# Kernel tuning notes

Measured on AMD Instinct MI355X. Metric: run time of the kernel, lower is better.

## Reference

```python
import jax, jax.numpy as jnp
import numpy as np

V, E, L, H = 128, 512, 8, 8
B, T = 4, 1024
EPS = 0.1  # label smoothing


def _ln(x, s, b):
    mu = x.mean(-1, keepdims=True)
    var = ((x - mu) ** 2).mean(-1, keepdims=True)
    return (x - mu) * jax.lax.rsqrt(var + 1e-5) * s + b


def _forward(inputs, targets, emb, qkv_w, qkv_b, aff1_w, aff1_b, aff2_w, aff2_b,
             ffn1_w, ffn1_b, ffn2_w, ffn2_b, ln1_s, ln1_b, ln2_s, ln2_b, head_w, head_b):
    Bx, Tx = inputs.shape
    x = emb[inputs]                                  # [B,T,E]
    dh = E // H
    mask = jnp.tril(jnp.ones((Tx, Tx), dtype=x.dtype))
    scale = np.float32(1.0 / np.sqrt(dh))
    for l in range(L):
        qkv = x @ qkv_w[l].T + qkv_b[l]              # [B,T,3E]
        qkv = qkv.reshape(Bx, Tx, H, 3 * dh).transpose(0, 2, 1, 3)  # [B,H,T,3dh]
        q, k, v = jnp.split(qkv, 3, axis=-1)
        # NOTE: original multiplies scores by boolean tril mask (zeros, not -inf)
        scores = jnp.einsum('bhqd,bhkd->bhqk', q, k) * mask * scale
        att = jax.nn.softmax(scores, axis=-1) @ v    # [B,H,T,dh]
        att = att.transpose(0, 2, 1, 3).reshape(Bx, Tx, E)
        att = jax.nn.relu(att @ aff1_w[l].T + aff1_b[l]) @ aff2_w[l].T + aff2_b[l]
        out1 = _ln(att + x, ln1_s[l], ln1_b[l])
        out2 = jax.nn.relu(out1 @ ffn1_w[l].T + ffn1_b[l]) @ ffn2_w[l].T + ffn2_b[l]
        x = _ln(out1 + out2, ln2_s[l], ln2_b[l])
    logits = x @ head_w.T + head_b                   # [B,T,V]
    logp = jax.nn.log_softmax(logits, axis=-1)
    nll = -jnp.take_along_axis(logp, targets[..., None], axis=-1)[..., 0]
    smooth = -logp.mean(-1)
    loss = jnp.mean((1.0 - EPS) * nll + EPS * smooth)
    return logits, loss


def setup_inputs() -> dict:
    key = jax.random.key(0)
    ks = jax.random.split(key, 16)
    s = lambda k, shape, fan: (jax.random.normal(k, shape, jnp.float32) / np.sqrt(fan)).astype(jnp.float32)
    return {
        'inputs': jax.random.randint(ks[0], (B, T), 0, V, dtype=jnp.int32).astype(jnp.int64),
        'targets': jax.random.randint(ks[1], (B, T), 0, V, dtype=jnp.int32).astype(jnp.int64),
        'emb': s(ks[2], (V, E), 1.0),
        'qkv_w': s(ks[3], (L, 3 * E, E), E),
        'qkv_b': jnp.zeros((L, 3 * E), jnp.float32),
        'aff1_w': s(ks[4], (L, E, E), E),
        'aff1_b': jnp.zeros((L, E), jnp.float32),
        'aff2_w': s(ks[5], (L, E, E), E),
        'aff2_b': jnp.zeros((L, E), jnp.float32),
        'ffn1_w': s(ks[6], (L, E, E), E),
        'ffn1_b': jnp.zeros((L, E), jnp.float32),
        'ffn2_w': s(ks[7], (L, E, E), E),
        'ffn2_b': jnp.zeros((L, E), jnp.float32),
        'ln1_s': jnp.ones((L, E), jnp.float32),
        'ln1_b': jnp.zeros((L, E), jnp.float32),
        'ln2_s': jnp.ones((L, E), jnp.float32),
        'ln2_b': jnp.zeros((L, E), jnp.float32),
        'head_w': s(ks[8], (V, E), E),
        'head_b': jnp.zeros((V,), jnp.float32),
    }


def reference(inputs, targets, emb, qkv_w, qkv_b, aff1_w, aff1_b, aff2_w, aff2_b,
              ffn1_w, ffn1_b, ffn2_w, ffn2_b, ln1_s, ln1_b, ln2_s, ln2_b, head_w, head_b):
    return _forward(inputs, targets, emb, qkv_w, qkv_b, aff1_w, aff1_b, aff2_w, aff2_b,
                    ffn1_w, ffn1_b, ffn2_w, ffn2_b, ln1_s, ln1_b, ln2_s, ln2_b, head_w, head_b)
```

## Files before the change

### kernel.cpp

```cpp
#include <hip/hip_runtime.h>


#define V_  128
#define E_  512
#define L_  8
#define H_  8
#define B_  4
#define T_  1024
#define N_  (B_*T_)
#define DH_ 64
#define E3_ 1536

typedef __attribute__((ext_vector_type(8))) short   bf16x8;
typedef __attribute__((ext_vector_type(4))) float   floatx4;

#define SW(row,k8) (((row) << 6) + ((((k8) ^ ((row) & 7))) << 3))

__device__ __forceinline__ unsigned short f2bf(float f) {
    union { float f; unsigned int i; } v; v.f = f;
    unsigned int x = v.i;
    return (unsigned short)((x + 0x7fffu + ((x >> 16) & 1u)) >> 16);
}
__device__ __forceinline__ float bf2f(unsigned short u) {
    union { unsigned int i; float f; } v; v.i = ((unsigned int)u) << 16; return v.f;
}
__device__ __forceinline__ void gload_lds16(const void* g, void* l) {
    __builtin_amdgcn_global_load_lds(
        (const __attribute__((address_space(1))) unsigned int*)g,
        (__attribute__((address_space(3))) unsigned int*)l, 16, 0, 0);
}

__device__ __forceinline__ void xcd_remap(int& mstrip, int& nblk) {
    int nx = gridDim.x;
    int flat = blockIdx.y * nx + blockIdx.x;
    int xcd = flat & 7;
    int j = flat >> 3;
    int per_xcd = gridDim.y >> 3;
    mstrip = xcd * per_xcd + j / nx;
    nblk = j % nx;
}

#define CVT_N0 6291456
#define CVT_N1 2097152
#define CVT_TOT (CVT_N0 + 4*CVT_N1 + V_*E_)
__global__ void cvt_all_kernel(const float* __restrict__ s0, const float* __restrict__ s1,
                               const float* __restrict__ s2, const float* __restrict__ s3,
                               const float* __restrict__ s4, const float* __restrict__ s5,
                               unsigned short* __restrict__ dst) {
    long i = (long)(blockIdx.x * blockDim.x + threadIdx.x) * 4;
    if (i >= CVT_TOT) return;
    const float* src; long off;
    if      (i < CVT_N0)               { src = s0; off = i; }
    else if (i < CVT_N0 + CVT_N1)      { src = s1; off = i - CVT_N0; }
    else if (i < CVT_N0 + 2*CVT_N1)    { src = s2; off = i - CVT_N0 - CVT_N1; }
    else if (i < CVT_N0 + 3*CVT_N1)    { src = s3; off = i - CVT_N0 - 2L*CVT_N1; }
    else if (i < CVT_N0 + 4*CVT_N1)    { src = s4; off = i - CVT_N0 - 3L*CVT_N1; }
    else                               { src = s5; off = i - CVT_N0 - 4L*CVT_N1; }
    float4 v = *(const float4*)(src + off);
    ushort4 o; o.x = f2bf(v.x); o.y = f2bf(v.y); o.z = f2bf(v.z); o.w = f2bf(v.w);
    *(ushort4*)(dst + i) = o;
}

__global__ void embed_kernel(const int* __restrict__ tok, const float* __restrict__ emb,
                             float* __restrict__ xf, unsigned short* __restrict__ xb) {
    int idx = blockIdx.x * blockDim.x + threadIdx.x;
    if (idx >= N_ * E_) return;
    int n = idx >> 9;
    int e = idx & (E_ - 1);
    float v = emb[tok[n] * E_ + e];
    xf[idx] = v; xb[idx] = f2bf(v);
}

template<int RELU, int WF, int WB, int ADDRES>
__global__ __launch_bounds__(256) void gemm64(
    const unsigned short* __restrict__ A, const unsigned short* __restrict__ W,
    const float* __restrict__ bias, const float* __restrict__ resF,
    float* __restrict__ Cf, unsigned short* __restrict__ Cb,
    int M, int Nout, int K)
{
    __shared__ unsigned short Asm[4][64 * 64];
    __shared__ unsigned short Bsm[4][64 * 64];
    int tid = threadIdx.x;
    int wv = tid >> 6, ln = tid & 63;
    int lquad = ln >> 4, lmod = ln & 15;
    int mh = wv & 1, kh = wv >> 1;
    int mstrip, nblk;
    xcd_remap(mstrip, nblk);
    int m0 = mstrip * 64, n0 = nblk * 64;

    floatx4 acc[2][4] = {};

    auto stage = [&](int k0, int s) {
        #pragma unroll
        for (int c = 0; c < 2; ++c) {
            int cc = tid + 256 * c;
            int r = cc >> 3, k8s = (cc & 7) ^ (r & 7);
            gload_lds16(A + (size_t)(m0 + r) * K + k0 + 8 * k8s,
                        &Asm[s][2048 * c + 512 * wv]);
        }
        #pragma unroll
        for (int c = 0; c < 2; ++c) {
            int cc = tid + 256 * c;
            int r = cc >> 3, k8s = (cc & 7) ^ (r & 7);
            gload_lds16(W + (size_t)(n0 + r) * K + k0 + 8 * k8s,
                        &Bsm[s][2048 * c + 512 * wv]);
        }
    };

    int np = K >> 7;
    stage(0, 0);
    stage(64, 1);
    __syncthreads();

    for (int t = 0; t < np; ++t) {
        if (t + 1 < np) {
            stage((2 * t + 2) << 6, (2 * t + 2) & 3);
            stage((2 * t + 3) << 6, (2 * t + 3) & 3);
        }
        #pragma unroll
        for (int half = 0; half < 2; ++half) {
            int s = (2 * t + half) & 3;
            bf16x8 af[2], bfr[4];
            #pragma unroll
            for (int i = 0; i < 2; ++i)
                af[i] = *(const bf16x8*)&Asm[s][SW(32 * mh + 16 * i + lmod, 4 * kh + lquad)];
            #pragma unroll
            for (int j = 0; j < 4; ++j)
                bfr[j] = *(const bf16x8*)&Bsm[s][SW(16 * j + lmod, 4 * kh + lquad)];
            #pragma unroll
            for (int i = 0; i < 2; ++i)
                #pragma unroll
                for (int j = 0; j < 4; ++j)
                    acc[i][j] = __builtin_amdgcn_mfma_f32_16x16x32_bf16(af[i], bfr[j], acc[i][j], 0, 0, 0);
        }
        if (t + 1 < np) __syncthreads();
    }

    float* redF = (float*)&Asm[0][0];
    if (kh == 1) {
        #pragma unroll
        for (int i = 0; i < 2; ++i)
            #pragma unroll
            for (int j = 0; j < 4; ++j) {
                int bidx = i * 4 + j;
                *(floatx4*)&redF[mh * 2048 + ln * 32 + (((bidx ^ (ln & 7))) << 2)] = acc[i][j];
            }
    }
    __syncthreads();
    if (kh == 0) {
        #pragma unroll
        for (int i = 0; i < 2; ++i)
            #pragma unroll
            for (int j = 0; j < 4; ++j) {
                int bidx = i * 4 + j;
                floatx4 part = *(const floatx4*)&redF[mh * 2048 + ln * 32 + (((bidx ^ (ln & 7))) << 2)];
                int n = n0 + 16 * j + lmod;
                float bj = bias[n];
                #pragma unroll
                for (int v = 0; v < 4; ++v) {
                    int m = m0 + 32 * mh + 16 * i + 4 * lquad + v;
                    float val = acc[i][j][v] + part[v] + bj;
                    if (ADDRES) val += resF[(size_t)m * Nout + n];
                    if (RELU) val = fmaxf(val, 0.f);
                    if (WF) Cf[(size_t)m * Nout + n] = val;
                    if (WB) Cb[(size_t)m * Nout + n] = f2bf(val);
                }
            }
    }
}

__global__ __launch_bounds__(256) void gemm_qkv(
    const unsigned short* __restrict__ A, const unsigned short* __restrict__ W,
    const float* __restrict__ bias, unsigned short* __restrict__ Cb,
    unsigned short* __restrict__ vt_g, float* __restrict__ vtile, int K)
{
    __shared__ unsigned short Asm[2][128 * 64];
    __shared__ unsigned short Bsm[2][64 * 64];
    __shared__ float vred[4][64];
    int tid = threadIdx.x;
    int wv = tid >> 6, ln = tid & 63;
    int lquad = ln >> 4, lmod = ln & 15;
    int mstrip, nblk;
    xcd_remap(mstrip, nblk);
    int m0 = mstrip * 128, n0 = nblk * 64;

    floatx4 acc[2][4] = {};

    auto stage = [&](int k0, int pb) {
        #pragma unroll
        for (int c = 0; c < 4; ++c) {
            int cc = tid + 256 * c;
            int r = cc >> 3, k8s = (cc & 7) ^ (r & 7);
            gload_lds16(A + (size_t)(m0 + r) * K + k0 + 8 * k8s,
                        &Asm[pb][2048 * c + 512 * wv]);
        }
        #pragma unroll
        for (int c = 0; c < 2; ++c) {
            int cc = tid + 256 * c;
            int r = cc >> 3, k8s = (cc & 7) ^ (r & 7);
            gload_lds16(W + (size_t)(n0 + r) * K + k0 + 8 * k8s,
                        &Bsm[pb][2048 * c + 512 * wv]);
        }
    };

    int nt = K >> 6;
    stage(0, 0);
    __syncthreads();
    for (int t = 0; t < nt; ++t) {
        int pb = t & 1;
        if (t + 1 < nt) stage((t + 1) << 6, pb ^ 1);
        #pragma unroll
        for (int ks = 0; ks < 2; ++ks) {
            bf16x8 af[2], bfr[4];
            #pragma unroll
            for (int i = 0; i < 2; ++i)
                af[i] = *(const bf16x8*)&Asm[pb][SW(32 * wv + 16 * i + lmod, ks * 4 + lquad)];
            #pragma unroll
            for (int j = 0; j < 4; ++j)
                bfr[j] = *(const bf16x8*)&Bsm[pb][SW(16 * j + lmod, ks * 4 + lquad)];
            #pragma unroll
            for (int i = 0; i < 2; ++i)
                #pragma unroll
                for (int j = 0; j < 4; ++j)
                    acc[i][j] = __builtin_amdgcn_mfma_f32_16x16x32_bf16(af[i], bfr[j], acc[i][j], 0, 0, 0);
        }
        if (t + 1 < nt) __syncthreads();
    }

    if ((n0 % 192) != 128) {
        #pragma unroll
        for (int i = 0; i < 2; ++i)
            #pragma unroll
            for (int j = 0; j < 4; ++j) {
                int n = n0 + 16 * j + lmod;
                float bj = bias[n];
                #pragma unroll
                for (int v = 0; v < 4; ++v) {
                    int m = m0 + 32 * wv + 16 * i + 4 * lquad + v;
                    Cb[(size_t)m * E3_ + n] = f2bf(acc[i][j][v] + bj);
                }
            }
    } else {
        int h = n0 / 192;
        int b = m0 >> 10;
        int bh = b * 8 + h;
        int t0 = m0 & 1023;
        int kt0 = t0 >> 6;
        float sj[4] = {0.f, 0.f, 0.f, 0.f};
        #pragma unroll
        for (int j = 0; j < 4; ++j) {
            float bj = bias[n0 + 16 * j + lmod];
            #pragma unroll
            for (int i = 0; i < 2; ++i) {
                union { unsigned short u[4]; uint2 q; } pk;
                #pragma unroll
                for (int v = 0; v < 4; ++v) {
                    unsigned short r = f2bf(acc[i][j][v] + bj);
                    pk.u[v] = r;
                    sj[j] += bf2f(r);
                }
                int t = t0 + 32 * wv + 16 * i + 4 * lquad;
                *(uint2*)&vt_g[((size_t)(bh * 64 + 16 * j + lmod)) * T_ + t] = pk.q;
            }
        }
        #pragma unroll
        for (int j = 0; j < 4; ++j) {
            sj[j] += __shfl_xor(sj[j], 16);
            sj[j] += __shfl_xor(sj[j], 32);
        }
        if (lquad == 0) {
            #pragma unroll
            for (int j = 0; j < 4; ++j) vred[wv][16 * j + lmod] = sj[j];
        }
        __syncthreads();
        if (tid < 128) {
            int half = tid >> 6, d = tid & 63;
            vtile[((size_t)bh * 16 + kt0 + half) * 64 + d] =
                vred[2 * half][d] + vred[2 * half + 1][d];
        }
    }
}

__global__ __launch_bounds__(256) void attn_mfma(const unsigned short* __restrict__ qkv,
                                                 const unsigned short* __restrict__ vt_g,
                                                 const float* __restrict__ vtile,
                                                 unsigned short* __restrict__ outb)
{
    __shared__ unsigned short Qs[64 * 64];
    __shared__ unsigned short Ks[2][64 * 64];
    __shared__ unsigned short Vs[2][64 * 64];
    __shared__ unsigned short Ps[64 * 64];

    int tid = threadIdx.x;
    int wv = tid >> 6, ln = tid & 63;
    int lquad = ln >> 4, lmod = ln & 15;
    int bh = blockIdx.x;
    int y = blockIdx.y;
    int qt = (y < 8) ? y : 23 - y;
    int b = bh >> 3, h = bh & 7;
    int q0 = qt * 64;
    const float scale = 0.125f;
    size_t base = (size_t)b * T_ * E3_ + h * 192;

    auto stageKV = [&](int k0, int pb) {
        #pragma unroll
        for (int c = 0; c < 2; ++c) {
            int cc = tid + 256 * c;
            int r = cc >> 3, k8s = (cc & 7) ^ (r & 7);
            gload_lds16(qkv + base + (size_t)(k0 + r) * E3_ + 64 + 8 * k8s,
                        &Ks[pb][2048 * c + 512 * wv]);
            gload_lds16(vt_g + ((size_t)(bh * 64 + r)) * T_ + k0 + 8 * k8s,
                        &Vs[pb][2048 * c + 512 * wv]);
        }
    };

    #pragma unroll
    for (int c = 0; c < 2; ++c) {
        int cc = tid + 256 * c;
        int r = cc >> 3, k8s = (cc & 7) ^ (r & 7);
        gload_lds16(qkv + base + (size_t)(q0 + r) * E3_ + 8 * k8s, Qs + 2048 * c + 512 * wv);
    }
    stageKV(0, 0);
    __syncthreads();

    float lrow[4] = {0.f, 0.f, 0.f, 0.f};
    floatx4 Oa[4] = {};

    for (int kt = 0; kt <= qt; ++kt) {
        int pb = kt & 1;
        int k0 = kt * 64;
        if (kt < qt) stageKV(k0 + 64, pb ^ 1);

        floatx4 sacc[4] = {};
        #pragma unroll
        for (int ks = 0; ks < 2; ++ks) {
            bf16x8 aq = *(const bf16x8*)&Qs[SW(16 * wv + lmod, ks * 4 + lquad)];
            #pragma unroll
            for (int j = 0; j < 4; ++j) {
                bf16x8 bk = *(const bf16x8*)&Ks[pb][SW(16 * j + lmod, ks * 4 + lquad)];
                sacc[j] = __builtin_amdgcn_mfma_f32_16x16x32_bf16(aq, bk, sacc[j], 0, 0, 0);
            }
        }
        #pragma unroll
        for (int v = 0; v < 4; ++v) {
            int qg = q0 + 16 * wv + 4 * lquad + v;
            int row = 16 * wv + 4 * lquad + v;
            #pragma unroll
            for (int j = 0; j < 4; ++j) {
                int kg = k0 + 16 * j + lmod;
                float p = (kg <= qg) ? __expf(sacc[j][v] * scale) : 1.0f;
                lrow[v] += p;
                int col = 16 * j + lmod;
                Ps[SW(row, col >> 3) + (col & 7)] = f2bf(p);
            }
        }
        asm volatile("s_waitcnt lgkmcnt(0)" ::: "memory");
        __builtin_amdgcn_sched_barrier(0);

        #pragma unroll
        for (int ks = 0; ks < 2; ++ks) {
            bf16x8 ap = *(const bf16x8*)&Ps[SW(16 * wv + lmod, ks * 4 + lquad)];
            #pragma unroll
            for (int f = 0; f < 4; ++f) {
                bf16x8 bv = *(const bf16x8*)&Vs[pb][SW(16 * f + lmod, ks * 4 + lquad)];
                Oa[f] = __builtin_amdgcn_mfma_f32_16x16x32_bf16(ap, bv, Oa[f], 0, 0, 0);
            }
        }
        if (kt < qt) __syncthreads();
    }

    #pragma unroll
    for (int v = 0; v < 4; ++v)
        #pragma unroll
        for (int msk = 1; msk < 16; msk <<= 1) lrow[v] += __shfl_xor(lrow[v], msk);

    if (qt < 15) {
        float Km = (float)((15 - qt) * 64);
        #pragma unroll
        for (int v = 0; v < 4; ++v) lrow[v] += Km;
        #pragma unroll
        for (int f = 0; f < 4; ++f) {
            float sv = 0.f;
            for (int kt = qt + 1; kt < 16; ++kt)
                sv += vtile[((size_t)bh * 16 + kt) * 64 + 16 * f + lmod];
            #pragma unroll
            for (int v = 0; v < 4; ++v) Oa[f][v] += sv;
        }
    }

    #pragma unroll
    for (int f = 0; f < 4; ++f)
        #pragma unroll
        for (int v = 0; v < 4; ++v) {
            int q = q0 + 16 * wv + 4 * lquad + v;
            outb[(size_t)(b * T_ + q) * E_ + h * DH_ + 16 * f + lmod] = f2bf(Oa[f][v] / lrow[v]);
        }
}

__global__ __launch_bounds__(256) void ln_kernel(
    const float* __restrict__ z,
    const float* __restrict__ s, const float* __restrict__ bpar,
    float* __restrict__ outF, unsigned short* __restrict__ outB)
{
    int tid = threadIdx.x, wv = tid >> 6, ln = tid & 63;
    int n = blockIdx.x * 4 + wv;
    int e = ln * 8;
    size_t base = (size_t)n * E_ + e;
    float4 a0 = *(const float4*)&z[base], a1 = *(const float4*)&z[base + 4];
    float v[8] = {a0.x, a0.y, a0.z, a0.w, a1.x, a1.y, a1.z, a1.w};

    float sm = 0.f;
    #pragma unroll
    for (int i = 0; i < 8; ++i) sm += v[i];
    #pragma unroll
    for (int msk = 1; msk < 64; msk <<= 1) sm += __shfl_xor(sm, msk);
    float mu = sm * (1.f / 512.f);

    float ss = 0.f;
    #pragma unroll
    for (int i = 0; i < 8; ++i) { v[i] -= mu; ss += v[i] * v[i]; }
    #pragma unroll
    for (int msk = 1; msk < 64; msk <<= 1) ss += __shfl_xor(ss, msk);
    float rstd = rsqrtf(ss * (1.f / 512.f) + 1e-5f);

    float4 sc0 = *(const float4*)&s[e],    sc1 = *(const float4*)&s[e + 4];
    float4 bp0 = *(const float4*)&bpar[e], bp1 = *(const float4*)&bpar[e + 4];
    float o[8];
    o[0] = v[0] * rstd * sc0.x + bp0.x; o[1] = v[1] * rstd * sc0.y + bp0.y;
    o[2] = v[2] * rstd * sc0.z + bp0.z; o[3] = v[3] * rstd * sc0.w + bp0.w;
    o[4] = v[4] * rstd * sc1.x + bp1.x; o[5] = v[5] * rstd * sc1.y + bp1.y;
    o[6] = v[6] * rstd * sc1.z + bp1.z; o[7] = v[7] * rstd * sc1.w + bp1.w;
    *(float4*)&outF[base]     = make_float4(o[0], o[1], o[2], o[3]);
    *(float4*)&outF[base + 4] = make_float4(o[4], o[5], o[6], o[7]);
    union { unsigned short u[8]; uint4 q; } pk;
    #pragma unroll
    for (int i = 0; i < 8; ++i) pk.u[i] = f2bf(o[i]);
    *(uint4*)&outB[base] = pk.q;
}

__global__ __launch_bounds__(256) void head_loss_kernel(
    const unsigned short* __restrict__ A, const unsigned short* __restrict__ W,
    const float* __restrict__ bias, const int* __restrict__ tgt,
    float* __restrict__ out_logits, float* __restrict__ rowloss)
{
    __shared__ unsigned short Asm[2][64 * 64];
    __shared__ unsigned short Bsm[2][128 * 64];
    int tid = threadIdx.x;
    int wv = tid >> 6, ln = tid & 63;
    int lquad = ln >> 4, lmod = ln & 15;
    int m0 = blockIdx.x * 64;

    floatx4 acc[8] = {};

    auto stage = [&](int k0, int pb) {
        #pragma unroll
        for (int c = 0; c < 2; ++c) {
            int cc = tid + 256 * c;
            int r = cc >> 3, k8s = (cc & 7) ^ (r & 7);
            gload_lds16(A + (size_t)(m0 + r) * E_ + k0 + 8 * k8s,
                        &Asm[pb][2048 * c + 512 * wv]);
        }
        #pragma unroll
        for (int c = 0; c < 4; ++c) {
            int cc = tid + 256 * c;
            int r = cc >> 3, k8s = (cc & 7) ^ (r & 7);
            gload_lds16(W + (size_t)r * E_ + k0 + 8 * k8s,
                        &Bsm[pb][2048 * c + 512 * wv]);
        }
    };

    stage(0, 0);
    __syncthreads();
    for (int t = 0; t < 8; ++t) {
        int pb = t & 1;
        if (t < 7) stage((t + 1) << 6, pb ^ 1);
        #pragma unroll
        for (int ks = 0; ks < 2; ++ks) {
            bf16x8 af = *(const bf16x8*)&Asm[pb][SW(16 * wv + lmod, ks * 4 + lquad)];
            #pragma unroll
            for (int j = 0; j < 8; ++j) {
                bf16x8 bf = *(const bf16x8*)&Bsm[pb][SW(16 * j + lmod, ks * 4 + lquad)];
                acc[j] = __builtin_amdgcn_mfma_f32_16x16x32_bf16(af, bf, acc[j], 0, 0, 0);
            }
        }
        if (t < 7) __syncthreads();
    }

    float bj[8];
    #pragma unroll
    for (int j = 0; j < 8; ++j) bj[j] = bias[16 * j + lmod];
    #pragma unroll
    for (int v = 0; v < 4; ++v) {
        int m = m0 + 16 * wv + 4 * lquad + v;
        float x[8];
        float mx = -1e30f, sx = 0.f;
        #pragma unroll
        for (int j = 0; j < 8; ++j) {
            x[j] = acc[j][v] + bj[j];
            out_logits[(size_t)m * V_ + 16 * j + lmod] = x[j];
            mx = fmaxf(mx, x[j]); sx += x[j];
        }
        #pragma unroll
        for (int msk = 1; msk < 16; msk <<= 1) mx = fmaxf(mx, __shfl_xor(mx, msk));
        float se = 0.f;
        #pragma unroll
        for (int j = 0; j < 8; ++j) se += __expf(x[j] - mx);
        #pragma unroll
        for (int msk = 1; msk < 16; msk <<= 1) {
            se += __shfl_xor(se, msk);
            sx += __shfl_xor(sx, msk);
        }
        int t = tgt[m];
        float cand = 0.f;
        #pragma unroll
        for (int j = 0; j < 8; ++j) cand = ((t >> 4) == j) ? x[j] : cand;
        float xt = __shfl(cand, (ln & 48) | (t & 15));
        if (lmod == 0) {
            float lse = mx + __logf(se);
            rowloss[m] = 0.9f * (lse - xt) + 0.1f * (lse - sx * (1.f / 128.f));
        }
    }
}

__global__ __launch_bounds__(256) void loss_reduce_kernel(
    const float* __restrict__ rowloss, float* __restrict__ out)
{
    int tid = threadIdx.x;
    float sm = 0.f;
    for (int idx = tid; idx < N_; idx += 256) sm += rowloss[idx];
    #pragma unroll
    for (int off = 32; off; off >>= 1) sm += __shfl_down(sm, off, 64);
    __shared__ float red[4];
    int lane = tid & 63, w = tid >> 6;
    if (lane == 0) red[w] = sm;
    __syncthreads();
    if (tid == 0) out[0] = (red[0] + red[1] + red[2] + red[3]) * (1.f / (float)N_);
}

extern "C" void kernel_launch(void* const* d_in, const int* in_sizes, int n_in,
                              void* d_out, int out_size, void* d_ws, size_t ws_size,
                              hipStream_t stream)
{
    (void)in_sizes; (void)n_in; (void)out_size; (void)ws_size;
    const int* toks     = (const int*)d_in[0];
    const int* tgts     = (const int*)d_in[1];
    const float* emb    = (const float*)d_in[2];
    const float* qkv_w  = (const float*)d_in[3];
    const float* qkv_b  = (const float*)d_in[4];
    const float* aff1_w = (const float*)d_in[5];
    const float* aff1_b = (const float*)d_in[6];
    const float* aff2_w = (const float*)d_in[7];
    const float* aff2_b = (const float*)d_in[8];
    const float* ffn1_w = (const float*)d_in[9];
    const float* ffn1_b = (const float*)d_in[10];
    const float* ffn2_w = (const float*)d_in[11];
    const float* ffn2_b = (const float*)d_in[12];
    const float* ln1_s  = (const float*)d_in[13];
    const float* ln1_b  = (const float*)d_in[14];
    const float* ln2_s  = (const float*)d_in[15];
    const float* ln2_b  = (const float*)d_in[16];
    const float* head_w = (const float*)d_in[17];
    const float* head_b = (const float*)d_in[18];

    char* p = (char*)d_ws;
    auto carve = [&](size_t bytes) { char* r = p; p += (bytes + 255) & ~(size_t)255; return (void*)r; };
    unsigned short* wb_all  = (unsigned short*)carve((size_t)CVT_TOT * 2);
    unsigned short* wb_qkv  = wb_all;
    unsigned short* wb_aff1 = wb_qkv  + (size_t)CVT_N0;
    unsigned short* wb_aff2 = wb_aff1 + (size_t)CVT_N1;
    unsigned short* wb_ffn1 = wb_aff2 + (size_t)CVT_N1;
    unsigned short* wb_ffn2 = wb_ffn1 + (size_t)CVT_N1;
    unsigned short* wb_head = wb_ffn2 + (size_t)CVT_N1;
    float*          x_f     = (float*)carve((size_t)N_ * E_ * 4);
    unsigned short* x_b     = (unsigned short*)carve((size_t)N_ * E_ * 2);
    unsigned short* qkv_bf  = (unsigned short*)carve((size_t)N_ * E3_ * 2);
    unsigned short* att_b   = (unsigned short*)carve((size_t)N_ * E_ * 2);
    unsigned short* h_b     = (unsigned short*)carve((size_t)N_ * E_ * 2);
    float*          y_f     = (float*)carve((size_t)N_ * E_ * 4);
    float*          o1_f    = (float*)carve((size_t)N_ * E_ * 4);
    unsigned short* o1_b    = (unsigned short*)carve((size_t)N_ * E_ * 2);
    float*          rowl    = (float*)carve((size_t)N_ * 4);
    float*          vtile   = (float*)carve((size_t)32 * 16 * 64 * 4);
    unsigned short* vt_g    = (unsigned short*)carve((size_t)32 * 64 * T_ * 2);

    float* out_logits = (float*)d_out;
    float* out_loss   = out_logits + (size_t)N_ * V_;

    cvt_all_kernel<<<dim3(CVT_TOT / 1024), 256, 0, stream>>>(
        qkv_w, aff1_w, aff2_w, ffn1_w, ffn2_w, head_w, wb_all);

    embed_kernel<<<dim3((N_ * E_) / 256), 256, 0, stream>>>(toks, emb, x_f, x_b);

    for (int l = 0; l < L_; ++l) {
        gemm_qkv<<<dim3(E3_/64, N_/128), 256, 0, stream>>>(
            x_b, wb_qkv + (size_t)l * E3_ * E_, qkv_b + (size_t)l * E3_,
            qkv_bf, vt_g, vtile, E_);
        attn_mfma<<<dim3(32, 16), 256, 0, stream>>>(qkv_bf, vt_g, vtile, att_b);
        gemm64<1,0,1,0><<<dim3(E_/64, N_/64), 256, 0, stream>>>(
            att_b, wb_aff1 + (size_t)l * E_ * E_, aff1_b + (size_t)l * E_,
            nullptr, nullptr, h_b, N_, E_, E_);
        gemm64<0,1,0,1><<<dim3(E_/64, N_/64), 256, 0, stream>>>(
            h_b, wb_aff2 + (size_t)l * E_ * E_, aff2_b + (size_t)l * E_,
            x_f, y_f, nullptr, N_, E_, E_);
        ln_kernel<<<dim3(N_/4), 256, 0, stream>>>(
            y_f, ln1_s + (size_t)l * E_, ln1_b + (size_t)l * E_, o1_f, o1_b);
        gemm64<1,0,1,0><<<dim3(E_/64, N_/64), 256, 0, stream>>>(
            o1_b, wb_ffn1 + (size_t)l * E_ * E_, ffn1_b + (size_t)l * E_,
            nullptr, nullptr, h_b, N_, E_, E_);
        gemm64<0,1,0,1><<<dim3(E_/64, N_/64), 256, 0, stream>>>(
            h_b, wb_ffn2 + (size_t)l * E_ * E_, ffn2_b + (size_t)l * E_,
            o1_f, y_f, nullptr, N_, E_, E_);
        ln_kernel<<<dim3(N_/4), 256, 0, stream>>>(
            y_f, ln2_s + (size_t)l * E_, ln2_b + (size_t)l * E_, x_f, x_b);
    }

    head_loss_kernel<<<dim3(N_/64), 256, 0, stream>>>(
        x_b, wb_head, head_b, tgts, out_logits, rowl);
    loss_reduce_kernel<<<dim3(1), 256, 0, stream>>>(rowl, out_loss);
}
```

Before: 780.6 us.

## Widen attention key tiles to 128 and split head GEMM K across waves

The attention kernel now processes 128-key tiles per iteration, with double-buffered K, a single V buffer and Q fragments hoisted into registers. This halves loop iterations and barriers. The masked-tail correction from the precomputed V sums starts at the next 128-aligned tile. The head/loss kernel uses 32-row blocks with the K dimension split between wave pairs and reduced through LDS, doubling the grid to improve occupancy. The trade-offs are more LDS per block and extra compute on the partially masked 128-wide diagonal tile.

Result: faster. 753.0 us (-3.5%).

```diff
diff --git a/kernel.cpp b/kernel.cpp
--- a/kernel.cpp
+++ b/kernel.cpp
@@ -15,6 +15,7 @@
 typedef __attribute__((ext_vector_type(4))) float   floatx4;
 
 #define SW(row,k8) (((row) << 6) + ((((k8) ^ ((row) & 7))) << 3))
+#define SW128(row,c) (((row) << 7) + ((((c) ^ ((row) & 7))) << 3))
 
 __device__ __forceinline__ unsigned short f2bf(float f) {
     union { float f; unsigned int i; } v; v.f = f;
@@ -287,9 +288,9 @@
                                                  unsigned short* __restrict__ outb)
 {
     __shared__ unsigned short Qs[64 * 64];
-    __shared__ unsigned short Ks[2][64 * 64];
-    __shared__ unsigned short Vs[2][64 * 64];
-    __shared__ unsigned short Ps[64 * 64];
+    __shared__ unsigned short Ks[2][128 * 64];
+    __shared__ unsigned short Vs[64 * 128];
+    __shared__ unsigned short Ps[64 * 128];
 
     int tid = threadIdx.x;
     int wv = tid >> 6, ln = tid & 63;
@@ -299,18 +300,27 @@
     int qt = (y < 8) ? y : 23 - y;
     int b = bh >> 3, h = bh & 7;
     int q0 = qt * 64;
+    int nt = (qt >> 1) + 1;
     const float scale = 0.125f;
     size_t base = (size_t)b * T_ * E3_ + h * 192;
 
-    auto stageKV = [&](int k0, int pb) {
-        #pragma unroll
-        for (int c = 0; c < 2; ++c) {
+    auto stageK = [&](int k0, int pb) {
+        #pragma unroll
+        for (int c = 0; c < 4; ++c) {
             int cc = tid + 256 * c;
             int r = cc >> 3, k8s = (cc & 7) ^ (r & 7);
             gload_lds16(qkv + base + (size_t)(k0 + r) * E3_ + 64 + 8 * k8s,
                         &Ks[pb][2048 * c + 512 * wv]);
+        }
+    };
+    auto stageV = [&](int k0) {
+        #pragma unroll
+        for (int c = 0; c < 4; ++c) {
+            int cc = tid + 256 * c;
+            int r = cc >> 4, c16 = cc & 15;
+            int k8s = c16 ^ (r & 7);
             gload_lds16(vt_g + ((size_t)(bh * 64 + r)) * T_ + k0 + 8 * k8s,
-                        &Vs[pb][2048 * c + 512 * wv]);
+                        &Vs[2048 * c + 512 * wv]);
         }
     };
 
@@ -320,53 +330,61 @@
         int r = cc >> 3, k8s = (cc & 7) ^ (r & 7);
         gload_lds16(qkv + base + (size_t)(q0 + r) * E3_ + 8 * k8s, Qs + 2048 * c + 512 * wv);
     }
-    stageKV(0, 0);
-    __syncthreads();
+    stageK(0, 0);
+    __syncthreads();
+
+    bf16x8 aq[2];
+    #pragma unroll
+    for (int ks = 0; ks < 2; ++ks)
+        aq[ks] = *(const bf16x8*)&Qs[SW(16 * wv + lmod, ks * 4 + lquad)];
 
     float lrow[4] = {0.f, 0.f, 0.f, 0.f};
     floatx4 Oa[4] = {};
 
-    for (int kt = 0; kt <= qt; ++kt) {
-        int pb = kt & 1;
-        int k0 = kt * 64;
-        if (kt < qt) stageKV(k0 + 64, pb ^ 1);
-
-        floatx4 sacc[4] = {};
-        #pragma unroll
-        for (int ks = 0; ks < 2; ++ks) {
-            bf16x8 aq = *(const bf16x8*)&Qs[SW(16 * wv + lmod, ks * 4 + lquad)];
-            #pragma unroll
-            for (int j = 0; j < 4; ++j) {
+    for (int t = 0; t < nt; ++t) {
+        int pb = t & 1;
+        int k0 = t * 128;
+        stageV(k0);
+        if (t + 1 < nt) stageK(k0 + 128, pb ^ 1);
+
+        floatx4 sacc[8] = {};
+        #pragma unroll
+        for (int ks = 0; ks < 2; ++ks)
+            #pragma unroll
+            for (int j = 0; j < 8; ++j) {
                 bf16x8 bk = *(const bf16x8*)&Ks[pb][SW(16 * j + lmod, ks * 4 + lquad)];
-                sacc[j] = __builtin_amdgcn_mfma_f32_16x16x32_bf16(aq, bk, sacc[j], 0, 0, 0);
-            }
-        }
+                sacc[j] = __builtin_amdgcn_mfma_f32_16x16x32_bf16(aq[ks], bk, sacc[j], 0, 0, 0);
+            }
+
         #pragma unroll
         for (int v = 0; v < 4; ++v) {
             int qg = q0 + 16 * wv + 4 * lquad + v;
             int row = 16 * wv + 4 * lquad + v;
             #pragma unroll
-            for (int j = 0; j < 4; ++j) {
+            for (int j = 0; j < 8; ++j) {
                 int kg = k0 + 16 * j + lmod;
                 float p = (kg <= qg) ? __expf(sacc[j][v] * scale) : 1.0f;
                 lrow[v] += p;
                 int col = 16 * j + lmod;
-                Ps[SW(row, col >> 3) + (col & 7)] = f2bf(p);
-            }
-        }
-        asm volatile("s_waitcnt lgkmcnt(0)" ::: "memory");
+                Ps[SW128(row, col >> 3) + (col & 7)] = f2bf(p);
+            }
+        }
+
+        if (t + 1 < nt) asm volatile("s_waitcnt vmcnt(4) lgkmcnt(0)" ::: "memory");
+        else            asm volatile("s_waitcnt vmcnt(0) lgkmcnt(0)" ::: "memory");
+        __builtin_amdgcn_s_barrier();
         __builtin_amdgcn_sched_barrier(0);
 
         #pragma unroll
-        for (int ks = 0; ks < 2; ++ks) {
-            bf16x8 ap = *(const bf16x8*)&Ps[SW(16 * wv + lmod, ks * 4 + lquad)];
+        for (int ks2 = 0; ks2 < 4; ++ks2) {
+            bf16x8 ap = *(const bf16x8*)&Ps[SW128(16 * wv + lmod, 4 * ks2 + lquad)];
             #pragma unroll
             for (int f = 0; f < 4; ++f) {
-                bf16x8 bv = *(const bf16x8*)&Vs[pb][SW(16 * f + lmod, ks * 4 + lquad)];
+                bf16x8 bv = *(const bf16x8*)&Vs[SW128(16 * f + lmod, 4 * ks2 + lquad)];
                 Oa[f] = __builtin_amdgcn_mfma_f32_16x16x32_bf16(ap, bv, Oa[f], 0, 0, 0);
             }
         }
-        if (kt < qt) __syncthreads();
+        if (t + 1 < nt) __syncthreads();
     }
 
     #pragma unroll
@@ -374,14 +392,15 @@
         #pragma unroll
         for (int msk = 1; msk < 16; msk <<= 1) lrow[v] += __shfl_xor(lrow[v], msk);
 
-    if (qt < 15) {
-        float Km = (float)((15 - qt) * 64);
+    int s0 = 2 * nt;
+    if (s0 < 16) {
+        float Km = (float)((16 - s0) * 64);
         #pragma unroll
         for (int v = 0; v < 4; ++v) lrow[v] += Km;
         #pragma unroll
         for (int f = 0; f < 4; ++f) {
             float sv = 0.f;
-            for (int kt = qt + 1; kt < 16; ++kt)
+            for (int kt = s0; kt < 16; ++kt)
                 sv += vtile[((size_t)bh * 16 + kt) * 64 + 16 * f + lmod];
             #pragma unroll
             for (int v = 0; v < 4; ++v) Oa[f][v] += sv;
@@ -443,22 +462,22 @@
     const float* __restrict__ bias, const int* __restrict__ tgt,
     float* __restrict__ out_logits, float* __restrict__ rowloss)
 {
-    __shared__ unsigned short Asm[2][64 * 64];
+    __shared__ unsigned short Asm[2][32 * 64];
     __shared__ unsigned short Bsm[2][128 * 64];
     int tid = threadIdx.x;
     int wv = tid >> 6, ln = tid & 63;
     int lquad = ln >> 4, lmod = ln & 15;
-    int m0 = blockIdx.x * 64;
+    int mh = wv & 1, kh = wv >> 1;
+    int m0 = blockIdx.x * 32;
 
     floatx4 acc[8] = {};
 
     auto stage = [&](int k0, int pb) {
-        #pragma unroll
-        for (int c = 0; c < 2; ++c) {
-            int cc = tid + 256 * c;
+        {
+            int cc = tid;
             int r = cc >> 3, k8s = (cc & 7) ^ (r & 7);
             gload_lds16(A + (size_t)(m0 + r) * E_ + k0 + 8 * k8s,
-                        &Asm[pb][2048 * c + 512 * wv]);
+                        &Asm[pb][512 * wv]);
         }
         #pragma unroll
         for (int c = 0; c < 4; ++c) {
@@ -474,50 +493,61 @@
     for (int t = 0; t < 8; ++t) {
         int pb = t & 1;
         if (t < 7) stage((t + 1) << 6, pb ^ 1);
-        #pragma unroll
-        for (int ks = 0; ks < 2; ++ks) {
-            bf16x8 af = *(const bf16x8*)&Asm[pb][SW(16 * wv + lmod, ks * 4 + lquad)];
+        bf16x8 af = *(const bf16x8*)&Asm[pb][SW(16 * mh + lmod, 4 * kh + lquad)];
+        #pragma unroll
+        for (int j = 0; j < 8; ++j) {
+            bf16x8 bf = *(const bf16x8*)&Bsm[pb][SW(16 * j + lmod, 4 * kh + lquad)];
+            acc[j] = __builtin_amdgcn_mfma_f32_16x16x32_bf16(af, bf, acc[j], 0, 0, 0);
+        }
+        if (t < 7) __syncthreads();
+    }
+
+    __syncthreads();
+    float* redF = (float*)&Bsm[0][0];
+    if (kh == 1) {
+        #pragma unroll
+        for (int j = 0; j < 8; ++j)
+            *(floatx4*)&redF[mh * 2048 + ln * 32 + (((j ^ (ln & 7))) << 2)] = acc[j];
+    }
+    __syncthreads();
+    if (kh == 0) {
+        float bj[8];
+        #pragma unroll
+        for (int j = 0; j < 8; ++j) bj[j] = bias[16 * j + lmod];
+        floatx4 part[8];
+        #pragma unroll
+        for (int j = 0; j < 8; ++j)
+            part[j] = *(const floatx4*)&redF[mh * 2048 + ln * 32 + (((j ^ (ln & 7))) << 2)];
+        #pragma unroll
+        for (int v = 0; v < 4; ++v) {
+            int m = m0 + 16 * mh + 4 * lquad + v;
+            float x[8];
+            float mx = -1e30f, sx = 0.f;
             #pragma unroll
             for (int j = 0; j < 8; ++j) {
-                bf16x8 bf = *(const bf16x8*)&Bsm[pb][SW(16 * j + lmod, ks * 4 + lquad)];
-                acc[j] = __builtin_amdgcn_mfma_f32_16x16x32_bf16(af, bf, acc[j], 0, 0, 0);
-            }
-        }
-        if (t < 7) __syncthreads();
-    }
-
-    float bj[8];
-    #pragma unroll
-    for (int j = 0; j < 8; ++j) bj[j] = bias[16 * j + lmod];
-    #pragma unroll
-    for (int v = 0; v < 4; ++v) {
-        int m = m0 + 16 * wv + 4 * lquad + v;
-        float x[8];
-        float mx = -1e30f, sx = 0.f;
-        #pragma unroll
-        for (int j = 0; j < 8; ++j) {
-            x[j] = acc[j][v] + bj[j];
-            out_logits[(size_t)m * V_ + 16 * j + lmod] = x[j];
-            mx = fmaxf(mx, x[j]); sx += x[j];
-        }
-        #pragma unroll
-        for (int msk = 1; msk < 16; msk <<= 1) mx = fmaxf(mx, __shfl_xor(mx, msk));
-        float se = 0.f;
-        #pragma unroll
-        for (int j = 0; j < 8; ++j) se += __expf(x[j] - mx);
-        #pragma unroll
-        for (int msk = 1; msk < 16; msk <<= 1) {
-            se += __shfl_xor(se, msk);
-            sx += __shfl_xor(sx, msk);
-        }
-        int t = tgt[m];
-        float cand = 0.f;
-        #pragma unroll
-        for (int j = 0; j < 8; ++j) cand = ((t >> 4) == j) ? x[j] : cand;
-        float xt = __shfl(cand, (ln & 48) | (t & 15));
-        if (lmod == 0) {
-            float lse = mx + __logf(se);
-            rowloss[m] = 0.9f * (lse - xt) + 0.1f * (lse - sx * (1.f / 128.f));
+                x[j] = acc[j][v] + part[j][v] + bj[j];
+                out_logits[(size_t)m * V_ + 16 * j + lmod] = x[j];
+                mx = fmaxf(mx, x[j]); sx += x[j];
+            }
+            #pragma unroll
+            for (int msk = 1; msk < 16; msk <<= 1) mx = fmaxf(mx, __shfl_xor(mx, msk));
+            float se = 0.f;
+            #pragma unroll
+            for (int j = 0; j < 8; ++j) se += __expf(x[j] - mx);
+            #pragma unroll
+            for (int msk = 1; msk < 16; msk <<= 1) {
+                se += __shfl_xor(se, msk);
+                sx += __shfl_xor(sx, msk);
+            }
+            int t = tgt[m];
+            float cand = 0.f;
+            #pragma unroll
+            for (int j = 0; j < 8; ++j) cand = ((t >> 4) == j) ? x[j] : cand;
+            float xt = __shfl(cand, (ln & 48) | (t & 15));
+            if (lmod == 0) {
+                float lse = mx + __logf(se);
+                rowloss[m] = 0.9f * (lse - xt) + 0.1f * (lse - sx * (1.f / 128.f));
+            }
         }
     }
 }
@@ -614,7 +644,7 @@
             y_f, ln2_s + (size_t)l * E_, ln2_b + (size_t)l * E_, x_f, x_b);
     }
 
-    head_loss_kernel<<<dim3(N_/64), 256, 0, stream>>>(
+    head_loss_kernel<<<dim3(N_/32), 256, 0, stream>>>(
         x_b, wb_head, head_b, tgts, out_logits, rowl);
     loss_reduce_kernel<<<dim3(1), 256, 0, stream>>>(rowl, out_loss);
 }
```
